# Kernel tuning notes

Measured on AMD Instinct MI355X. Metric: run time of the kernel, lower is better.

## Reference

```python
import jax, jax.numpy as jnp
import numpy as np

N_NODES = 50000
N_EDGES = 800000
IN_DIM = 128
HID_DIM = 128
OUT_DIM = 64


def setup_inputs() -> dict:
    key = jax.random.key(0)
    ks = jax.random.split(key, 6)
    x = jax.random.normal(ks[0], (N_NODES, IN_DIM), dtype=jnp.float32)
    edge_index = jax.random.randint(ks[1], (2, N_EDGES), 0, N_NODES, dtype=jnp.int64)
    # per-hop linear weights (torch Linear layout: [out, in], no bias)
    s = 1.0 / np.sqrt(IN_DIM)
    W0 = jax.random.uniform(ks[2], (HID_DIM, IN_DIM), jnp.float32, -s, s)
    W1 = jax.random.uniform(ks[3], (HID_DIM, IN_DIM), jnp.float32, -s, s)
    W2 = jax.random.uniform(ks[4], (HID_DIM, IN_DIM), jnp.float32, -s, s)
    s2 = 1.0 / np.sqrt(HID_DIM * 3)
    Wfc = jax.random.uniform(ks[5], (OUT_DIM, HID_DIM * 3), jnp.float32, -s2, s2)
    return {"x": x, "edge_index": edge_index, "W0": W0, "W1": W1, "W2": W2, "Wfc": Wfc}


def reference(x, edge_index, W0, W1, W2, Wfc):
    N = x.shape[0]
    row, col = edge_index[0], edge_index[1]  # source, target (PyG source_to_target flow)
    # symmetric degree normalization based on in-degree (degree(col, N))
    deg = jax.ops.segment_sum(jnp.ones(row.shape[0], dtype=x.dtype), col, num_segments=N)
    deg_inv_sqrt = jnp.where(deg > 0, jax.lax.rsqrt(jnp.where(deg > 0, deg, 1.0)), 0.0)
    norm = deg_inv_sqrt[row] * deg_inv_sqrt[col]  # [E]
    # NOTE: original code propagates the ORIGINAL x each iteration, so hops 1 and 2
    # both see the 1-hop propagation of x. Faithfully reproduced here.
    px = jax.ops.segment_sum(norm[:, None] * x[row], col, num_segments=N)  # [N, IN_DIM]
    # per-hop linear projections, concat over hops p=[0,1,2]
    h = jnp.concatenate([x @ W0.T, px @ W1.T, px @ W2.T], axis=1)  # [N, 3*HID_DIM]
    return h @ Wfc.T  # [N, OUT_DIM]
```

## Files before the change

### kernel.cpp

```cpp
#include <hip/hip_runtime.h>
#include <hip/hip_bf16.h>

#define N_IN  128
#define N_OUT 64
#define FB    32
#define MAXNBF 1568
#define CHUNK 4096
#define PADR  136
#define SLACK 1024

typedef __attribute__((ext_vector_type(8))) short short8;
typedef __attribute__((ext_vector_type(4))) float floatx4;

__device__ __forceinline__ unsigned pack_bf16(float a, float b) {
    __hip_bfloat16 ba = __float2bfloat16(a);
    __hip_bfloat16 bb = __float2bfloat16(b);
    unsigned short ua = *(unsigned short*)&ba;
    unsigned short ub = *(unsigned short*)&bb;
    return ((unsigned)ub << 16) | ua;
}
__device__ __forceinline__ float blo(unsigned u) { return __uint_as_float(u << 16); }
__device__ __forceinline__ float bhi(unsigned u) { return __uint_as_float(u & 0xffff0000u); }

__global__ void prep_kernel(const float* __restrict__ W0,
                            const float* __restrict__ W1,
                            const float* __restrict__ W2,
                            const float* __restrict__ Wfc,
                            __hip_bfloat16* __restrict__ CT,
                            int* __restrict__ gcur, int NBF) {
    int t = blockIdx.x * blockDim.x + threadIdx.x;
    if (t < NBF) gcur[t] = t * SLACK;
    if (t >= 128 * 128) return;
    int n = t >> 7;
    int i = t & 127;
    float a = 0.f;
    if (n < 64) {
        for (int k = 0; k < 128; ++k)
            a += Wfc[n * 384 + k] * W0[k * N_IN + i];
    } else {
        int o = n - 64;
        for (int k = 0; k < 128; ++k)
            a += Wfc[o * 384 + 128 + k] * W1[k * N_IN + i]
               + Wfc[o * 384 + 256 + k] * W2[k * N_IN + i];
    }
    CT[t] = __float2bfloat16(a);
}

__global__ __launch_bounds__(256) void fill_scatter(const int* __restrict__ ei,
                                                    int* __restrict__ gcur,
                                                    unsigned* __restrict__ gsorted,
                                                    int E, int NBF) {
    __shared__ int lcnt[MAXNBF];
    __shared__ int gbase_s[MAXNBF];
    int base = blockIdx.x * CHUNK;
    for (int i = threadIdx.x; i < NBF; i += 256) lcnt[i] = 0;
    __syncthreads();
    int myc[CHUNK / 256];
    #pragma unroll
    for (int q = 0; q < CHUNK / 256; ++q) {
        int e = base + q * 256 + threadIdx.x;
        int c = (e < E) ? ei[E + e] : -1;
        myc[q] = c;
        if (c >= 0) atomicAdd(&lcnt[c >> 5], 1);
    }
    __syncthreads();
    for (int f = threadIdx.x; f < NBF; f += 256) {
        int n = lcnt[f];
        gbase_s[f] = (n > 0) ? atomicAdd(&gcur[f], n) : 0;
    }
    __syncthreads();
    #pragma unroll
    for (int q = 0; q < CHUNK / 256; ++q) {
        int c = myc[q];
        if (c >= 0) {
            int e = base + q * 256 + threadIdx.x;
            unsigned r = (unsigned)ei[e];
            int p = atomicAdd(&gbase_s[c >> 5], 1);
            if (p < ((c >> 5) + 1) * SLACK)
                gsorted[p] = ((unsigned)c << 16) | r;
        }
    }
}

__global__ __launch_bounds__(256) void sortgemm_kernel(
        const int* __restrict__ gcur,
        const unsigned* __restrict__ gsorted,
        unsigned short* __restrict__ srow,
        int* __restrict__ offs,
        int* __restrict__ cnt,
        float* __restrict__ dis,
        const float* __restrict__ x,
        const __hip_bfloat16* __restrict__ CT,
        float* __restrict__ out,
        __hip_bfloat16* __restrict__ z,
        int N, int NBF) {
    __shared__ __align__(16) char smem[(64 + 128) * PADR * 2];
    int tid = threadIdx.x;

    if (blockIdx.x < NBF) {
        int* c32 = (int*)smem;
        int* b32 = c32 + FB;
        int* cur = b32 + FB;
        int f = blockIdx.x;
        int lo = f * SLACK;
        int m = min(gcur[f] - lo, SLACK);
        if (tid < FB) c32[tid] = 0;
        __syncthreads();
        for (int i = tid; i < m; i += 256) {
            int cl = (gsorted[lo + i] >> 16) & (FB - 1);
            atomicAdd(&c32[cl], 1);
        }
        __syncthreads();
        if (tid == 0) {
            int s = 0;
            for (int t = 0; t < FB; ++t) { b32[t] = s; cur[t] = s; s += c32[t]; }
        }
        __syncthreads();
        if (tid < FB) {
            int node = f * FB + tid;
            if (node < N) {
                int c = c32[tid];
                offs[node] = lo + b32[tid];
                cnt[node] = c;
                dis[node] = c > 0 ? rsqrtf((float)c) : 0.f;
            }
        }
        for (int i = tid; i < m; i += 256) {
            unsigned val = gsorted[lo + i];
            int cl = (val >> 16) & (FB - 1);
            int p = atomicAdd(&cur[cl], 1);
            srow[lo + p] = (unsigned short)(val & 0xffffu);
        }
        return;
    }

    unsigned short* xs = (unsigned short*)smem;
    unsigned short* Bs = xs + 64 * PADR;
    int base = (blockIdx.x - NBF) * 64;

    {
        int row = tid >> 2;
        int colq = (tid & 3) * 32;
        int node = base + row;
        unsigned tmp[16];
        if (node < N) {
            const float4* src = (const float4*)(x + (size_t)node * N_IN + colq);
            #pragma unroll
            for (int q = 0; q < 8; ++q) {
                float4 v = src[q];
                tmp[q * 2]     = pack_bf16(v.x, v.y);
                tmp[q * 2 + 1] = pack_bf16(v.z, v.w);
            }
        } else {
            #pragma unroll
            for (int q = 0; q < 16; ++q) tmp[q] = 0u;
        }
        unsigned* dst = (unsigned*)(xs + row * PADR + colq);
        #pragma unroll
        for (int q = 0; q < 16; ++q) dst[q] = tmp[q];
    }
    {
        const unsigned* src = (const unsigned*)CT;
        for (int c = tid; c < 8192; c += 256) {
            int row = c >> 6;
            int col = (c & 63) * 2;
            *(unsigned*)(Bs + row * PADR + col) = src[c];
        }
    }
    __syncthreads();

    int wave = tid >> 6, lane = tid & 63;
    int wm = wave & 1, wn = wave >> 1;
    int quad = lane >> 4, l16 = lane & 15;

    floatx4 acc[2][4];
    #pragma unroll
    for (int mt = 0; mt < 2; ++mt)
        #pragma unroll
        for (int nt = 0; nt < 4; ++nt)
            acc[mt][nt] = (floatx4){0.f, 0.f, 0.f, 0.f};

    #pragma unroll
    for (int kc = 0; kc < 4; ++kc) {
        int kof = kc * 32 + quad * 8;
        short8 afr[2], bfr[4];
        #pragma unroll
        for (int mt = 0; mt < 2; ++mt)
            afr[mt] = *(const short8*)(xs + (wm * 32 + mt * 16 + l16) * PADR + kof);
        #pragma unroll
        for (int nt = 0; nt < 4; ++nt)
            bfr[nt] = *(const short8*)(Bs + (wn * 64 + nt * 16 + l16) * PADR + kof);
        #pragma unroll
        for (int mt = 0; mt < 2; ++mt)
            #pragma unroll
            for (int nt = 0; nt < 4; ++nt)
                acc[mt][nt] = __builtin_amdgcn_mfma_f32_16x16x32_bf16(
                    afr[mt], bfr[nt], acc[mt][nt], 0, 0, 0);
    }

    #pragma unroll
    for (int mt = 0; mt < 2; ++mt) {
        #pragma unroll
        for (int reg = 0; reg < 4; ++reg) {
            int node = base + wm * 32 + mt * 16 + quad * 4 + reg;
            if (node >= N) continue;
            if (wn == 0) {
                #pragma unroll
                for (int nt = 0; nt < 4; ++nt)
                    out[(size_t)node * N_OUT + nt * 16 + l16] = acc[mt][nt][reg];
            } else {
                #pragma unroll
                for (int nt = 0; nt < 4; ++nt)
                    z[((size_t)node << 6) + nt * 16 + l16] =
                        __float2bfloat16(acc[mt][nt][reg]);
            }
        }
    }
}

__global__ __launch_bounds__(256) void gather_kernel(
        const int* __restrict__ offs, const int* __restrict__ cnt,
        const unsigned short* __restrict__ srow, const __hip_bfloat16* __restrict__ z,
        const float* __restrict__ dis, float* __restrict__ out, int N) {
    int node = blockIdx.x * 4 + (threadIdx.x >> 6);
    if (node >= N) return;
    int lane = threadIdx.x & 63;
    int sub  = lane >> 3;
    int jj   = lane & 7;
    int start = offs[node];
    int deg   = cnt[node];
    float a[8] = {0.f, 0.f, 0.f, 0.f, 0.f, 0.f, 0.f, 0.f};
    for (int k0 = 0; k0 < deg; k0 += 64) {
        int m = min(64, deg - k0);
        int idx = 0; float dv = 0.f;
        if (lane < m) {
            idx = (int)srow[start + k0 + lane];
            dv = dis[idx];
        }
        for (int kk = 0; kk < m; kk += 16) {
            int s0 = kk + sub, s1 = kk + 8 + sub;
            int r0 = __shfl(idx, s0); float d0 = __shfl(dv, s0);
            int r1 = __shfl(idx, s1); float d1 = __shfl(dv, s1);
            uint4 u0 = make_uint4(0u, 0u, 0u, 0u), u1 = make_uint4(0u, 0u, 0u, 0u);
            if (s0 < m) u0 = ((const uint4*)(z + ((size_t)r0 << 6)))[jj];
            if (s1 < m) u1 = ((const uint4*)(z + ((size_t)r1 << 6)))[jj];
            a[0] += d0 * blo(u0.x) + d1 * blo(u1.x);
            a[1] += d0 * bhi(u0.x) + d1 * bhi(u1.x);
            a[2] += d0 * blo(u0.y) + d1 * blo(u1.y);
            a[3] += d0 * bhi(u0.y) + d1 * bhi(u1.y);
            a[4] += d0 * blo(u0.z) + d1 * blo(u1.z);
            a[5] += d0 * bhi(u0.z) + d1 * bhi(u1.z);
            a[6] += d0 * blo(u0.w) + d1 * blo(u1.w);
            a[7] += d0 * bhi(u0.w) + d1 * bhi(u1.w);
        }
    }
    #pragma unroll
    for (int q = 0; q < 8; ++q) {
        a[q] += __shfl_xor(a[q], 8);
        a[q] += __shfl_xor(a[q], 16);
        a[q] += __shfl_xor(a[q], 32);
    }
    if (lane < 8 && deg > 0) {
        float dn = dis[node];
        float4* op = (float4*)(out + ((size_t)node << 6) + jj * 8);
        float4 o0 = op[0], o1 = op[1];
        o0.x += dn * a[0]; o0.y += dn * a[1]; o0.z += dn * a[2]; o0.w += dn * a[3];
        o1.x += dn * a[4]; o1.y += dn * a[5]; o1.z += dn * a[6]; o1.w += dn * a[7];
        op[0] = o0; op[1] = o1;
    }
}

extern "C" void kernel_launch(void* const* d_in, const int* in_sizes, int n_in,
                              void* d_out, int out_size, void* d_ws, size_t ws_size,
                              hipStream_t stream) {
    const float* x   = (const float*)d_in[0];
    const int*   ei  = (const int*)d_in[1];
    const float* W0  = (const float*)d_in[2];
    const float* W1  = (const float*)d_in[3];
    const float* W2  = (const float*)d_in[4];
    const float* Wfc = (const float*)d_in[5];
    float* out = (float*)d_out;
    int N = in_sizes[0] / N_IN;
    int E = in_sizes[1] / 2;
    int NBF = (N + FB - 1) / FB;
    int GB  = (N + 63) / 64;

    __hip_bfloat16* CT = (__hip_bfloat16*)d_ws;
    int*   cnt     = (int*)((char*)d_ws + 32768);
    float* dis     = (float*)(cnt + N);
    int*   gcur    = (int*)(dis + N);
    int*   offs    = gcur + NBF;
    unsigned* gsorted = (unsigned*)(offs + N);
    unsigned short* srow = (unsigned short*)(gsorted + (size_t)NBF * SLACK);
    size_t zoff = ((size_t)(srow + (size_t)NBF * SLACK) - (size_t)d_ws + 15) & ~(size_t)15;
    __hip_bfloat16* z = (__hip_bfloat16*)((char*)d_ws + zoff);

    prep_kernel<<<64, 256, 0, stream>>>(W0, W1, W2, Wfc, CT, gcur, NBF);
    fill_scatter<<<(E + CHUNK - 1) / CHUNK, 256, 0, stream>>>(ei, gcur, gsorted, E, NBF);
    sortgemm_kernel<<<NBF + GB, 256, 0, stream>>>(gcur, gsorted, srow, offs, cnt, dis,
                                                  x, CT, out, z, N, NBF);
    gather_kernel<<<(N + 3) / 4, 256, 0, stream>>>(offs, cnt, srow, z, dis, out, N);
}
```

Baseline: 153.5 us.

## Coarsen edge bucketing to 256-node buckets with LDS-staged counting sort

Edges are now bucketed by destination into coarse 256-node groups instead of 32-node groups. Each sort block stages its bucket in shared memory and computes per-node offsets with a parallel prefix scan. This cuts the number of buckets and the global atomic traffic per scatter block, and avoids re-reading gsorted from global memory. The cost is much larger per-block sort work (about 4k edges), fewer sort blocks, and a fixed slack of 5120 per bucket that silently drops edges if a bucket overflows.

```diff
diff --git a/kernel.cpp b/kernel.cpp
--- a/kernel.cpp
+++ b/kernel.cpp
@@ -3,11 +3,11 @@
 
 #define N_IN  128
 #define N_OUT 64
-#define FB    32
-#define MAXNBF 1568
-#define CHUNK 4096
-#define PADR  136
-#define SLACK 1024
+#define CFB    256
+#define MAXNBC 200
+#define SLACKC 5120
+#define CHUNK  2048
+#define PADR   136
 
 typedef __attribute__((ext_vector_type(8))) short short8;
 typedef __attribute__((ext_vector_type(4))) float floatx4;
@@ -27,9 +27,9 @@
                             const float* __restrict__ W2,
                             const float* __restrict__ Wfc,
                             __hip_bfloat16* __restrict__ CT,
-                            int* __restrict__ gcur, int NBF) {
+                            int* __restrict__ gcur, int NBC) {
     int t = blockIdx.x * blockDim.x + threadIdx.x;
-    if (t < NBF) gcur[t] = t * SLACK;
+    if (t < NBC) gcur[t] = t * SLACKC;
     if (t >= 128 * 128) return;
     int n = t >> 7;
     int i = t & 127;
@@ -49,11 +49,11 @@
 __global__ __launch_bounds__(256) void fill_scatter(const int* __restrict__ ei,
                                                     int* __restrict__ gcur,
                                                     unsigned* __restrict__ gsorted,
-                                                    int E, int NBF) {
-    __shared__ int lcnt[MAXNBF];
-    __shared__ int gbase_s[MAXNBF];
+                                                    int E, int NBC) {
+    __shared__ int lcnt[MAXNBC];
+    __shared__ int gbase_s[MAXNBC];
     int base = blockIdx.x * CHUNK;
-    for (int i = threadIdx.x; i < NBF; i += 256) lcnt[i] = 0;
+    for (int i = threadIdx.x; i < NBC; i += 256) lcnt[i] = 0;
     __syncthreads();
     int myc[CHUNK / 256];
     #pragma unroll
@@ -61,10 +61,10 @@
         int e = base + q * 256 + threadIdx.x;
         int c = (e < E) ? ei[E + e] : -1;
         myc[q] = c;
-        if (c >= 0) atomicAdd(&lcnt[c >> 5], 1);
+        if (c >= 0) atomicAdd(&lcnt[c >> 8], 1);
     }
     __syncthreads();
-    for (int f = threadIdx.x; f < NBF; f += 256) {
+    for (int f = threadIdx.x; f < NBC; f += 256) {
         int n = lcnt[f];
         gbase_s[f] = (n > 0) ? atomicAdd(&gcur[f], n) : 0;
     }
@@ -75,8 +75,8 @@
         if (c >= 0) {
             int e = base + q * 256 + threadIdx.x;
             unsigned r = (unsigned)ei[e];
-            int p = atomicAdd(&gbase_s[c >> 5], 1);
-            if (p < ((c >> 5) + 1) * SLACK)
+            int p = atomicAdd(&gbase_s[c >> 8], 1);
+            if (p < ((c >> 8) + 1) * SLACKC)
                 gsorted[p] = ((unsigned)c << 16) | r;
         }
     }
@@ -93,41 +93,46 @@
         const __hip_bfloat16* __restrict__ CT,
         float* __restrict__ out,
         __hip_bfloat16* __restrict__ z,
-        int N, int NBF) {
+        int N, int NBC) {
     __shared__ __align__(16) char smem[(64 + 128) * PADR * 2];
     int tid = threadIdx.x;
 
-    if (blockIdx.x < NBF) {
-        int* c32 = (int*)smem;
-        int* b32 = c32 + FB;
-        int* cur = b32 + FB;
+    if (blockIdx.x < NBC) {
+        unsigned* ev = (unsigned*)smem;
+        int* c256 = (int*)(smem + SLACKC * 4);
+        int* cur  = c256 + 256;
+        int* ts   = cur + 256;
         int f = blockIdx.x;
-        int lo = f * SLACK;
-        int m = min(gcur[f] - lo, SLACK);
-        if (tid < FB) c32[tid] = 0;
+        int lo = f * SLACKC;
+        int m = min(gcur[f] - lo, SLACKC);
+        for (int i = tid; i < m; i += 256) ev[i] = gsorted[lo + i];
+        c256[tid] = 0;
+        __syncthreads();
+        for (int i = tid; i < m; i += 256)
+            atomicAdd(&c256[(ev[i] >> 16) & (CFB - 1)], 1);
+        __syncthreads();
+        int v = c256[tid];
+        int xx = v;
+        ts[tid] = xx;
+        __syncthreads();
+        for (int off = 1; off < 256; off <<= 1) {
+            int t2 = (tid >= off) ? ts[tid - off] : 0;
+            __syncthreads();
+            xx += t2; ts[tid] = xx;
+            __syncthreads();
+        }
+        int b = xx - v;
+        cur[tid] = b;
+        int node = f * CFB + tid;
+        if (node < N) {
+            offs[node] = lo + b;
+            cnt[node] = v;
+            dis[node] = v > 0 ? rsqrtf((float)v) : 0.f;
+        }
         __syncthreads();
         for (int i = tid; i < m; i += 256) {
-            int cl = (gsorted[lo + i] >> 16) & (FB - 1);
-            atomicAdd(&c32[cl], 1);
-        }
-        __syncthreads();
-        if (tid == 0) {
-            int s = 0;
-            for (int t = 0; t < FB; ++t) { b32[t] = s; cur[t] = s; s += c32[t]; }
-        }
-        __syncthreads();
-        if (tid < FB) {
-            int node = f * FB + tid;
-            if (node < N) {
-                int c = c32[tid];
-                offs[node] = lo + b32[tid];
-                cnt[node] = c;
-                dis[node] = c > 0 ? rsqrtf((float)c) : 0.f;
-            }
-        }
-        for (int i = tid; i < m; i += 256) {
-            unsigned val = gsorted[lo + i];
-            int cl = (val >> 16) & (FB - 1);
+            unsigned val = ev[i];
+            int cl = (val >> 16) & (CFB - 1);
             int p = atomicAdd(&cur[cl], 1);
             srow[lo + p] = (unsigned short)(val & 0xffffu);
         }
@@ -136,7 +141,7 @@
 
     unsigned short* xs = (unsigned short*)smem;
     unsigned short* Bs = xs + 64 * PADR;
-    int base = (blockIdx.x - NBF) * 64;
+    int base = (blockIdx.x - NBC) * 64;
 
     {
         int row = tid >> 2;
@@ -282,22 +287,22 @@
     float* out = (float*)d_out;
     int N = in_sizes[0] / N_IN;
     int E = in_sizes[1] / 2;
-    int NBF = (N + FB - 1) / FB;
+    int NBC = (N + CFB - 1) / CFB;
     int GB  = (N + 63) / 64;
 
     __hip_bfloat16* CT = (__hip_bfloat16*)d_ws;
     int*   cnt     = (int*)((char*)d_ws + 32768);
     float* dis     = (float*)(cnt + N);
     int*   gcur    = (int*)(dis + N);
-    int*   offs    = gcur + NBF;
+    int*   offs    = gcur + NBC;
     unsigned* gsorted = (unsigned*)(offs + N);
-    unsigned short* srow = (unsigned short*)(gsorted + (size_t)NBF * SLACK);
-    size_t zoff = ((size_t)(srow + (size_t)NBF * SLACK) - (size_t)d_ws + 15) & ~(size_t)15;
+    unsigned short* srow = (unsigned short*)(gsorted + (size_t)NBC * SLACKC);
+    size_t zoff = ((size_t)(srow + (size_t)NBC * SLACKC) - (size_t)d_ws + 15) & ~(size_t)15;
     __hip_bfloat16* z = (__hip_bfloat16*)((char*)d_ws + zoff);
 
-    prep_kernel<<<64, 256, 0, stream>>>(W0, W1, W2, Wfc, CT, gcur, NBF);
-    fill_scatter<<<(E + CHUNK - 1) / CHUNK, 256, 0, stream>>>(ei, gcur, gsorted, E, NBF);
-    sortgemm_kernel<<<NBF + GB, 256, 0, stream>>>(gcur, gsorted, srow, offs, cnt, dis,
-                                                  x, CT, out, z, N, NBF);
+    prep_kernel<<<64, 256, 0, stream>>>(W0, W1, W2, Wfc, CT, gcur, NBC);
+    fill_scatter<<<(E + CHUNK - 1) / CHUNK, 256, 0, stream>>>(ei, gcur, gsorted, E, NBC);
+    sortgemm_kernel<<<NBC + GB, 256, 0, stream>>>(gcur, gsorted, srow, offs, cnt, dis,
+                                                  x, CT, out, z, N, NBC);
     gather_kernel<<<(N + 3) / 4, 256, 0, stream>>>(offs, cnt, srow, z, dis, out, N);
 }
```

New measurement: 148.0 us. -3.5%, faster.
